# Optimization experiments

Hardware: AMD Instinct MI355X
Metric: run time of the kernel (lower is better)

## Reference

```python
import jax, jax.numpy as jnp
import numpy as np

N = 100_000   # nodes
E = 1_600_000 # edges per edge type
DIN = 128     # input_dim
DH = 128      # prot_hidden_dim
L = 3         # prot_num_layers
EPS = 1e-5


def setup_inputs() -> dict:
    key = jax.random.key(0)
    ks = jax.random.split(key, 8)
    s = 1.0 / np.sqrt(DH)
    return {
        "x": jax.random.normal(ks[0], (N, DIN), jnp.float32),
        "src": jax.random.randint(ks[1], (3, E), 0, N, jnp.int32),
        "dst": jax.random.randint(ks[2], (3, E), 0, N, jnp.int32),
        "gc_W0": jax.random.normal(ks[3], (3, DIN, DH), jnp.float32) * s,
        "gc_b0": jnp.zeros((3, DH), jnp.float32),
        "gc_W": jax.random.normal(ks[4], (L - 1, 3, DH, DH), jnp.float32) * s,
        "gc_b": jnp.zeros((L - 1, 3, DH), jnp.float32),
        "fc_W": jax.random.normal(ks[5], (L, DH, DH), jnp.float32) * s,
        "fc_b": jnp.zeros((L, DH), jnp.float32),
        "bn_gamma": jnp.ones((L, DH), jnp.float32),
        "bn_beta": jnp.zeros((L, DH), jnp.float32),
    }


def _graph_conv(x, src, dst, W, b):
    # DGL GraphConv, norm='both': D_in^{-1/2} A D_out^{-1/2} X W + b
    ones = jnp.ones(src.shape[0], x.dtype)
    deg_out = jnp.clip(jax.ops.segment_sum(ones, src, num_segments=N), 1.0)
    deg_in = jnp.clip(jax.ops.segment_sum(ones, dst, num_segments=N), 1.0)
    # apply weight first (same math; keeps gathered message width = DH)
    h = (x * jax.lax.rsqrt(deg_out)[:, None]) @ W  # [N, DH]
    agg = jax.ops.segment_sum(h[src], dst, num_segments=N)  # gather + scatter-add
    return agg * jax.lax.rsqrt(deg_in)[:, None] + b


def _batchnorm(x, gamma, beta):
    # training-mode BatchNorm1d: biased batch statistics
    mu = jnp.mean(x, axis=0)
    var = jnp.mean(jnp.square(x - mu), axis=0)
    return (x - mu) * jax.lax.rsqrt(var + EPS) * gamma + beta


def reference(x, src, dst, gc_W0, gc_b0, gc_W, gc_b, fc_W, fc_b, bn_gamma, bn_beta):
    h = x
    for l in range(L):
        W = gc_W0 if l == 0 else gc_W[l - 1]
        b = gc_b0 if l == 0 else gc_b[l - 1]
        # HeteroGraphConv with aggregate='sum' over 3 edge types
        out = _graph_conv(h, src[0], dst[0], W[0], b[0])
        for e in range(1, 3):
            out = out + _graph_conv(h, src[e], dst[e], W[e], b[e])
        # FC -> ReLU -> BatchNorm (dropout = identity in eval mode)
        h = _batchnorm(jax.nn.relu(out @ fc_W[l] + fc_b[l]), bn_gamma[l], bn_beta[l])
    return h
```

## Files before the change

### kernel.cpp

```cpp
#include <hip/hip_runtime.h>


#define EPSV 1e-5f
#define CH 4096
#define MAXNB 512

typedef __attribute__((ext_vector_type(8))) short s8v;
typedef __attribute__((ext_vector_type(4))) float f4v;

__global__ void coarse_hist(const int* __restrict__ src, const int* __restrict__ dst,
                            int* __restrict__ chd, int* __restrict__ chs,
                            int E, int NB) {
    __shared__ int hd[MAXNB], hs[MAXNB];
    int t = blockIdx.y;
    for (int i = threadIdx.x; i < MAXNB; i += 256) { hd[i] = 0; hs[i] = 0; }
    __syncthreads();
    int base = blockIdx.x * CH;
    int end = base + CH < E ? base + CH : E;
    const int* sp = src + (size_t)t * E;
    const int* dp = dst + (size_t)t * E;
    for (int i = base + threadIdx.x; i < end; i += 256) {
        atomicAdd(&hd[dp[i] >> 8], 1);
        atomicAdd(&hs[sp[i] >> 8], 1);
    }
    __syncthreads();
    for (int b = threadIdx.x; b < NB; b += 256) {
        if (hd[b]) atomicAdd(&chd[t * NB + b], hd[b]);
        if (hs[b]) atomicAdd(&chs[t * NB + b], hs[b]);
    }
}

__global__ void scan_off(const int* __restrict__ chd, const int* __restrict__ chs,
                         int* __restrict__ offd, int* __restrict__ offs,
                         int* __restrict__ gcd, int* __restrict__ gcs,
                         int* __restrict__ rowptr, int NB, int N, int E) {
    __shared__ int s[MAXNB];
    int tid = threadIdx.x;
    for (int a = 0; a < 6; ++a) {
        const int* h = (a < 3) ? chd + a * NB : chs + (a - 3) * NB;
        int* off = (a < 3) ? offd + a * (NB + 1) : offs + (a - 3) * (NB + 1);
        int* gc = (a < 3) ? gcd + a * NB : gcs + (a - 3) * NB;
        s[tid] = (tid < NB) ? h[tid] : 0;
        __syncthreads();
        for (int o = 1; o < MAXNB; o <<= 1) {
            int v = (tid >= o) ? s[tid - o] : 0;
            __syncthreads();
            s[tid] += v;
            __syncthreads();
        }
        if (tid < NB) {
            off[tid + 1] = s[tid];
            if (tid == 0) off[0] = 0;
        }
        __syncthreads();
        if (tid < NB) gc[tid] = off[tid];
        __syncthreads();
    }
    if (tid < 3) rowptr[tid * (N + 1) + N] = E;
}

__launch_bounds__(256)
__global__ void scatter_coarse(const int* __restrict__ src, const int* __restrict__ dst,
                               int* __restrict__ gcd, int* __restrict__ gcs,
                               int* __restrict__ dbuf, unsigned char* __restrict__ sbuf,
                               int E, int NB) {
    __shared__ int hd[MAXNB], hs[MAXNB];
    __shared__ int lod[MAXNB], los[MAXNB];
    __shared__ int bd[MAXNB], bs[MAXNB];
    __shared__ int rbi[CH];
    __shared__ unsigned char rbs[CH];
    const int tid = threadIdx.x;
    const int t = blockIdx.y;
    const int base = blockIdx.x * CH;
    const int end = base + CH < E ? base + CH : E;
    const int cnt = end - base;
    const int* sp = src + (size_t)t * E;
    const int* dp = dst + (size_t)t * E;

    for (int i = tid; i < MAXNB; i += 256) { hd[i] = 0; hs[i] = 0; }
    __syncthreads();
    for (int i = base + tid; i < end; i += 256) {
        atomicAdd(&hd[dp[i] >> 8], 1);
        atomicAdd(&hs[sp[i] >> 8], 1);
    }
    __syncthreads();
    for (int b = tid; b < NB; b += 256) {
        bd[b] = hd[b] ? atomicAdd(&gcd[t * NB + b], hd[b]) : 0;
        bs[b] = hs[b] ? atomicAdd(&gcs[t * NB + b], hs[b]) : 0;
    }
    lod[tid] = hd[tid]; lod[tid + 256] = hd[tid + 256];
    los[tid] = hs[tid]; los[tid + 256] = hs[tid + 256];
    __syncthreads();
    for (int o = 1; o < MAXNB; o <<= 1) {
        int a0 = lod[tid], a1 = lod[tid + 256];
        int b0 = los[tid], b1 = los[tid + 256];
        int p0 = (tid >= o) ? lod[tid - o] : 0;
        int p1 = lod[tid + 256 - o];
        int q0 = (tid >= o) ? los[tid - o] : 0;
        int q1 = los[tid + 256 - o];
        __syncthreads();
        lod[tid] = a0 + p0; lod[tid + 256] = a1 + p1;
        los[tid] = b0 + q0; los[tid + 256] = b1 + q1;
        __syncthreads();
    }
    hd[tid] = lod[tid] - hd[tid]; hd[tid + 256] = lod[tid + 256] - hd[tid + 256];
    hs[tid] = los[tid] - hs[tid]; hs[tid + 256] = los[tid + 256] - hs[tid + 256];
    __syncthreads();
    for (int i = base + tid; i < end; i += 256) {
        int sv = sp[i], dv = dp[i];
        int lp = atomicAdd(&hd[dv >> 8], 1);
        rbi[lp] = (sv << 8) | (dv & 255);
        int ls = atomicAdd(&hs[sv >> 8], 1);
        rbs[ls] = (unsigned char)(sv & 255);
    }
    __syncthreads();
    for (int i = tid; i < cnt; i += 256) {
        int lo = 0, hi = NB - 1;
        while (lo < hi) { int mid = (lo + hi) >> 1; if (lod[mid] > i) hi = mid; else lo = mid + 1; }
        int excl = lo ? lod[lo - 1] : 0;
        dbuf[(size_t)t * E + bd[lo] + (i - excl)] = rbi[i];
    }
    for (int i = tid; i < cnt; i += 256) {
        int lo = 0, hi = NB - 1;
        while (lo < hi) { int mid = (lo + hi) >> 1; if (los[mid] > i) hi = mid; else lo = mid + 1; }
        int excl = lo ? los[lo - 1] : 0;
        sbuf[(size_t)t * E + bs[lo] + (i - excl)] = rbs[i];
    }
}

__global__ void fine_src(const unsigned char* __restrict__ sbuf, const int* __restrict__ offs,
                         float* __restrict__ dro, int E, int N, int NB) {
    __shared__ int h[256];
    int b = blockIdx.x, t = blockIdx.y;
    int tid = threadIdx.x;
    h[tid] = 0;
    __syncthreads();
    int beg = offs[t * (NB + 1) + b], end = offs[t * (NB + 1) + b + 1];
    const unsigned char* sp = sbuf + (size_t)t * E;
    for (int i = beg + tid; i < end; i += 256) atomicAdd(&h[sp[i]], 1);
    __syncthreads();
    int node = b * 256 + tid;
    if (node < N) {
        int dg = h[tid] < 1 ? 1 : h[tid];
        dro[(size_t)t * N + node] = rsqrtf((float)dg);
    }
}

#define FDCAP 6656
__global__ void fine_dst(const int* __restrict__ dbuf, const int* __restrict__ offd,
                         const float* __restrict__ dro, int2* __restrict__ esrcw,
                         int* __restrict__ rowptr, float* __restrict__ dri,
                         int E, int N, int NB) {
    __shared__ int h[256], sc[256], cur[256];
    __shared__ int rb[FDCAP];
    int b = blockIdx.x, t = blockIdx.y;
    int tid = threadIdx.x;
    h[tid] = 0;
    __syncthreads();
    int beg = offd[t * (NB + 1) + b], end = offd[t * (NB + 1) + b + 1];
    int cnt = end - beg;
    const int* dp = dbuf + (size_t)t * E;
    const float* drt = dro + (size_t)t * N;
    for (int i = beg + tid; i < end; i += 256) atomicAdd(&h[dp[i] & 255], 1);
    __syncthreads();
    sc[tid] = h[tid];
    __syncthreads();
    for (int o = 1; o < 256; o <<= 1) {
        int v = (tid >= o) ? sc[tid - o] : 0;
        __syncthreads();
        sc[tid] += v;
        __syncthreads();
    }
    int excl = sc[tid] - h[tid];
    cur[tid] = excl;
    int node = b * 256 + tid;
    if (node < N) {
        rowptr[t * (N + 1) + node] = beg + excl;
        int dg = h[tid] < 1 ? 1 : h[tid];
        dri[(size_t)t * N + node] = rsqrtf((float)dg);
    }
    __syncthreads();
    if (cnt <= FDCAP) {
        for (int i = beg + tid; i < end; i += 256) {
            int v = dp[i];
            int p = atomicAdd(&cur[v & 255], 1);
            rb[p] = v >> 8;
        }
        __syncthreads();
        for (int i = tid; i < cnt; i += 256) {
            int sv = rb[i];
            esrcw[(size_t)t * E + beg + i] = make_int2(sv, __float_as_int(drt[sv]));
        }
    } else {
        for (int i = beg + tid; i < end; i += 256) {
            int v = dp[i];
            int sv = v >> 8;
            int p = beg + atomicAdd(&cur[v & 255], 1);
            esrcw[(size_t)t * E + p] = make_int2(sv, __float_as_int(drt[sv]));
        }
    }
}

__device__ __forceinline__ unsigned int bfr(float f) {
    unsigned int u = __float_as_uint(f);
    return (u + 0x7FFFu + ((u >> 16) & 1u)) >> 16;
}
__device__ __forceinline__ unsigned int pack2(float lo, float hi) {
    return bfr(lo) | (bfr(hi) << 16);
}
__device__ __forceinline__ float blo(unsigned int u) { return __uint_as_float(u << 16); }
__device__ __forceinline__ float bhi(unsigned int u) { return __uint_as_float(u & 0xFFFF0000u); }

__global__ void cvt_bf16(const float* __restrict__ h, unsigned short* __restrict__ h2,
                         int total8) {
    int i = blockIdx.x * 256 + threadIdx.x;
    if (i >= total8) return;
    const float4* hp = (const float4*)h + (size_t)i * 2;
    float4 v0 = hp[0], v1 = hp[1];
    uint4 o;
    o.x = pack2(v0.x, v0.y);
    o.y = pack2(v0.z, v0.w);
    o.z = pack2(v1.x, v1.y);
    o.w = pack2(v1.z, v1.w);
    ((uint4*)h2)[i] = o;
}

__global__ void pack_w(const float* __restrict__ gcW0, const float* __restrict__ gcW,
                       const float* __restrict__ fcW, unsigned short* __restrict__ Wg,
                       unsigned short* __restrict__ Wf) {
    int mat = blockIdx.x;
    const float* srcp;
    unsigned short* dstp;
    if (mat < 9) {
        int l = mat / 3, e = mat % 3;
        srcp = (l == 0) ? gcW0 + (size_t)e * 16384
                        : gcW + ((size_t)(l - 1) * 3 + e) * 16384;
        dstp = Wg + (size_t)mat * 16384;
    } else {
        srcp = fcW + (size_t)(mat - 9) * 16384;
        dstp = Wf + (size_t)(mat - 9) * 16384;
    }
    for (int p = threadIdx.x; p < 16384; p += 256) {
        int j = p & 7;
        int ln = (p >> 3) & 63;
        int nt = (p >> 9) & 7;
        int ks = p >> 12;
        int k = ks * 32 + (ln >> 4) * 8 + j;
        int n = nt * 16 + (ln & 15);
        dstp[p] = (unsigned short)bfr(srcp[k * 128 + n]);
    }
}

template <int AFF>
__launch_bounds__(256)
__global__ void agg_kernel(const unsigned short* __restrict__ h2, const int* __restrict__ rowptrB,
                           const int2* __restrict__ esrcwB, const float* __restrict__ driB,
                           const float* __restrict__ bnsum, const float* __restrict__ gamma,
                           const float* __restrict__ beta, float invn,
                           unsigned short* __restrict__ zB, int N, int E) {
    __shared__ float lss[256];
    if (AFF) {
        int tid = threadIdx.x;
        if (tid < 128) {
            float mean = bnsum[tid] * invn;
            float var = bnsum[128 + tid] * invn - mean * mean;
            float sc = gamma[tid] * rsqrtf(var + EPSV);
            lss[tid] = sc;
            lss[128 + tid] = beta[tid] - mean * sc;
        }
        __syncthreads();
    }
    const int e = blockIdx.y;
    const int* rowptr = rowptrB + e * (N + 1);
    const int2* esrcw = esrcwB + (size_t)e * E;
    const float* dri = driB + (size_t)e * N;
    unsigned short* z = zB + (size_t)e * N * 128;

    int idx = blockIdx.x * 256 + threadIdx.x;
    int node = idx >> 4;
    int lq = idx & 15;
    if (node >= N) return;
    int beg = rowptr[node], end = rowptr[node + 1];
    const uint4* hp = (const uint4*)h2 + lq;
    float a0 = 0.f, a1 = 0.f, a2 = 0.f, a3 = 0.f, a4 = 0.f, a5 = 0.f, a6 = 0.f, a7 = 0.f;
    float wacc = 0.f;
    int j = beg;
    for (; j + 8 <= end; j += 8) {
        int2 r[8];
#pragma unroll
        for (int q = 0; q < 8; ++q) r[q] = esrcw[j + q];
        uint4 u[8];
#pragma unroll
        for (int q = 0; q < 8; ++q) u[q] = hp[(size_t)r[q].x * 16];
#pragma unroll
        for (int q = 0; q < 8; ++q) {
            float w = __int_as_float(r[q].y);
            if (AFF) wacc += w;
            a0 += w * blo(u[q].x); a1 += w * bhi(u[q].x);
            a2 += w * blo(u[q].y); a3 += w * bhi(u[q].y);
            a4 += w * blo(u[q].z); a5 += w * bhi(u[q].z);
            a6 += w * blo(u[q].w); a7 += w * bhi(u[q].w);
        }
    }
    for (; j + 4 <= end; j += 4) {
        int2 r[4];
#pragma unroll
        for (int q = 0; q < 4; ++q) r[q] = esrcw[j + q];
        uint4 u[4];
#pragma unroll
        for (int q = 0; q < 4; ++q) u[q] = hp[(size_t)r[q].x * 16];
#pragma unroll
        for (int q = 0; q < 4; ++q) {
            float w = __int_as_float(r[q].y);
            if (AFF) wacc += w;
            a0 += w * blo(u[q].x); a1 += w * bhi(u[q].x);
            a2 += w * blo(u[q].y); a3 += w * bhi(u[q].y);
            a4 += w * blo(u[q].z); a5 += w * bhi(u[q].z);
            a6 += w * blo(u[q].w); a7 += w * bhi(u[q].w);
        }
    }
    for (; j < end; ++j) {
        int2 r0 = esrcw[j];
        float w = __int_as_float(r0.y);
        if (AFF) wacc += w;
        uint4 u0 = hp[(size_t)r0.x * 16];
        a0 += w * blo(u0.x); a1 += w * bhi(u0.x);
        a2 += w * blo(u0.y); a3 += w * bhi(u0.y);
        a4 += w * blo(u0.z); a5 += w * bhi(u0.z);
        a6 += w * blo(u0.w); a7 += w * bhi(u0.w);
    }
    float scl = dri[node];
    if (AFF) {
        const float* ap = &lss[lq * 8];
        const float* bp = &lss[128 + lq * 8];
        a0 = ap[0] * a0 + bp[0] * wacc;
        a1 = ap[1] * a1 + bp[1] * wacc;
        a2 = ap[2] * a2 + bp[2] * wacc;
        a3 = ap[3] * a3 + bp[3] * wacc;
        a4 = ap[4] * a4 + bp[4] * wacc;
        a5 = ap[5] * a5 + bp[5] * wacc;
        a6 = ap[6] * a6 + bp[6] * wacc;
        a7 = ap[7] * a7 + bp[7] * wacc;
    }
    uint4 o;
    o.x = pack2(a0 * scl, a1 * scl);
    o.y = pack2(a2 * scl, a3 * scl);
    o.z = pack2(a4 * scl, a5 * scl);
    o.w = pack2(a6 * scl, a7 * scl);
    ((uint4*)z)[(size_t)node * 16 + lq] = o;
}

__launch_bounds__(256)
__global__ void mfma_gc(const unsigned short* __restrict__ zB,
                        const unsigned short* __restrict__ Wp,
                        const float* __restrict__ b3,
                        unsigned short* __restrict__ C, int M) {
    const int tid = threadIdx.x;
    const int l = tid & 63;
    const int wv = tid >> 6;
    const int wm = wv >> 1, wn = wv & 1;
    const int m0 = blockIdx.x * 128;
    const int lr = l & 15;
    const int lk = (l >> 4) * 8;
    f4v acc[4][4];
#pragma unroll
    for (int i = 0; i < 4; ++i)
#pragma unroll
        for (int j = 0; j < 4; ++j) acc[i][j] = (f4v){0.f, 0.f, 0.f, 0.f};

    int rowb[4];
#pragma unroll
    for (int mt = 0; mt < 4; ++mt) {
        int r = m0 + wm * 64 + mt * 16 + lr;
        rowb[mt] = (r < M) ? r : (M - 1);
    }
#pragma unroll
    for (int e = 0; e < 3; ++e) {
        const unsigned short* zp = zB + (size_t)e * M * 128;
        const unsigned short* wp = Wp + (size_t)e * 16384;
#pragma unroll
        for (int ks = 0; ks < 4; ++ks) {
            s8v a[4], b[4];
#pragma unroll
            for (int mt = 0; mt < 4; ++mt)
                a[mt] = *(const s8v*)(zp + (size_t)rowb[mt] * 128 + ks * 32 + lk);
#pragma unroll
            for (int nt = 0; nt < 4; ++nt)
                b[nt] = *(const s8v*)(wp + ks * 4096 + (wn * 4 + nt) * 512 + l * 8);
#pragma unroll
            for (int mt = 0; mt < 4; ++mt)
#pragma unroll
                for (int nt = 0; nt < 4; ++nt)
                    acc[mt][nt] = __builtin_amdgcn_mfma_f32_16x16x32_bf16(
                        a[mt], b[nt], acc[mt][nt], 0, 0, 0);
        }
    }
    float bs[4];
    int col[4];
#pragma unroll
    for (int nt = 0; nt < 4; ++nt) {
        col[nt] = wn * 64 + nt * 16 + lr;
        bs[nt] = b3[col[nt]] + b3[128 + col[nt]] + b3[256 + col[nt]];
    }
#pragma unroll
    for (int mt = 0; mt < 4; ++mt) {
#pragma unroll
        for (int r = 0; r < 4; ++r) {
            int row = m0 + wm * 64 + mt * 16 + (l >> 4) * 4 + r;
            if (row < M) {
                unsigned short* cp = C + (size_t)row * 128;
#pragma unroll
                for (int nt = 0; nt < 4; ++nt)
                    cp[col[nt]] = (unsigned short)bfr(acc[mt][nt][r] + bs[nt]);
            }
        }
    }
}

template <int MODE>
__launch_bounds__(256)
__global__ void mfma_fc(const unsigned short* __restrict__ A,
                        const unsigned short* __restrict__ Wp,
                        const float* __restrict__ bias,
                        unsigned short* __restrict__ outb, float* __restrict__ outf,
                        float* __restrict__ bnsum, int M) {
    __shared__ float red[256];
    const int tid = threadIdx.x;
    const int l = tid & 63;
    const int wv = tid >> 6;
    const int wm = wv >> 1, wn = wv & 1;
    const int m0 = blockIdx.x * 128;
    const int lr = l & 15;
    const int lk = (l >> 4) * 8;
    f4v acc[4][4];
#pragma unroll
    for (int i = 0; i < 4; ++i)
#pragma unroll
        for (int j = 0; j < 4; ++j) acc[i][j] = (f4v){0.f, 0.f, 0.f, 0.f};

    int rowb[4];
#pragma unroll
    for (int mt = 0; mt < 4; ++mt) {
        int r = m0 + wm * 64 + mt * 16 + lr;
        rowb[mt] = (r < M) ? r : (M - 1);
    }
#pragma unroll
    for (int ks = 0; ks < 4; ++ks) {
        s8v a[4], b[4];
#pragma unroll
        for (int mt = 0; mt < 4; ++mt)
            a[mt] = *(const s8v*)(A + (size_t)rowb[mt] * 128 + ks * 32 + lk);
#pragma unroll
        for (int nt = 0; nt < 4; ++nt)
            b[nt] = *(const s8v*)(Wp + ks * 4096 + (wn * 4 + nt) * 512 + l * 8);
#pragma unroll
        for (int mt = 0; mt < 4; ++mt)
#pragma unroll
            for (int nt = 0; nt < 4; ++nt)
                acc[mt][nt] = __builtin_amdgcn_mfma_f32_16x16x32_bf16(
                    a[mt], b[nt], acc[mt][nt], 0, 0, 0);
    }

    float bv[4], cs[4] = {}, cq[4] = {};
    int col[4];
#pragma unroll
    for (int nt = 0; nt < 4; ++nt) {
        col[nt] = wn * 64 + nt * 16 + lr;
        bv[nt] = bias[col[nt]];
    }
#pragma unroll
    for (int mt = 0; mt < 4; ++mt) {
#pragma unroll
        for (int r = 0; r < 4; ++r) {
            int row = m0 + wm * 64 + mt * 16 + (l >> 4) * 4 + r;
            if (row < M) {
#pragma unroll
                for (int nt = 0; nt < 4; ++nt) {
                    float v = acc[mt][nt][r] + bv[nt];
                    v = v > 0.f ? v : 0.f;
                    cs[nt] += v;
                    cq[nt] += v * v;
                    if (MODE == 0)
                        outb[(size_t)row * 128 + col[nt]] = (unsigned short)bfr(v);
                    else
                        outf[(size_t)row * 128 + col[nt]] = v;
                }
            }
        }
    }
    red[tid] = 0.f;
    __syncthreads();
#pragma unroll
    for (int nt = 0; nt < 4; ++nt) {
        atomicAdd(&red[col[nt]], cs[nt]);
        atomicAdd(&red[128 + col[nt]], cq[nt]);
    }
    __syncthreads();
    if (tid < 128) {
        atomicAdd(&bnsum[tid], red[tid]);
        atomicAdd(&bnsum[128 + tid], red[128 + tid]);
    }
}

__global__ void bn_apply(float* __restrict__ h, const float* __restrict__ bnsum,
                         const float* __restrict__ gamma, const float* __restrict__ beta,
                         float invn, int total4) {
    __shared__ float lss[256];
    int tid = threadIdx.x;
    if (tid < 128) {
        float mean = bnsum[tid] * invn;
        float var = bnsum[128 + tid] * invn - mean * mean;
        float sc = gamma[tid] * rsqrtf(var + EPSV);
        lss[tid] = sc;
        lss[128 + tid] = beta[tid] - mean * sc;
    }
    __syncthreads();
    int i = blockIdx.x * 256 + tid;
    if (i >= total4) return;
    int c4 = (i & 31) * 4;
    float4 sc = *(const float4*)&lss[c4];
    float4 sh = *(const float4*)&lss[128 + c4];
    float4 v = ((float4*)h)[i];
    v.x = v.x * sc.x + sh.x;
    v.y = v.y * sc.y + sh.y;
    v.z = v.z * sc.z + sh.z;
    v.w = v.w * sc.w + sh.w;
    ((float4*)h)[i] = v;
}

extern "C" void kernel_launch(void* const* d_in, const int* in_sizes, int n_in,
                              void* d_out, int out_size, void* d_ws, size_t ws_size,
                              hipStream_t stream) {
    const float* x    = (const float*)d_in[0];
    const int*   src  = (const int*)d_in[1];
    const int*   dst  = (const int*)d_in[2];
    const float* gcW0 = (const float*)d_in[3];
    const float* gcb0 = (const float*)d_in[4];
    const float* gcW  = (const float*)d_in[5];
    const float* gcb  = (const float*)d_in[6];
    const float* fcW  = (const float*)d_in[7];
    const float* fcb  = (const float*)d_in[8];
    const float* bng  = (const float*)d_in[9];
    const float* bnb  = (const float*)d_in[10];
    float* out = (float*)d_out;

    const int N = in_sizes[0] / 128;
    const int E = in_sizes[1] / 3;
    const int NB = (N + 255) / 256;

    char* w = (char*)d_ws;
    auto alloc = [&](size_t bytes) -> char* {
        char* p = w;
        w += (bytes + 255) & ~(size_t)255;
        return p;
    };
    unsigned short* zB    = (unsigned short*)alloc((size_t)3 * N * 128 * 2);
    unsigned short* gcout = (unsigned short*)alloc((size_t)N * 128 * 2);
    unsigned short* h2    = (unsigned short*)alloc((size_t)N * 128 * 2);
    unsigned short* Wg    = (unsigned short*)alloc((size_t)9 * 16384 * 2);
    unsigned short* Wf    = (unsigned short*)alloc((size_t)3 * 16384 * 2);
    int2*  esrcw  = (int2*)alloc((size_t)3 * E * 8);
    int*   rowptr = (int*)alloc((size_t)3 * (N + 1) * 4);
    float* dro    = (float*)alloc((size_t)3 * N * 4);
    float* dri    = (float*)alloc((size_t)3 * N * 4);
    int*   chd    = (int*)alloc((size_t)3 * NB * 4);
    int*   chs    = (int*)alloc((size_t)3 * NB * 4);
    int*   offd   = (int*)alloc((size_t)3 * (NB + 1) * 4);
    int*   offs   = (int*)alloc((size_t)3 * (NB + 1) * 4);
    int*   gcd    = (int*)alloc((size_t)3 * NB * 4);
    int*   gcs    = (int*)alloc((size_t)3 * NB * 4);
    float* bnsum  = (float*)alloc(256 * 4);
    int* dbuf = (int*)zB;
    unsigned char* sbuf = (unsigned char*)gcout;

    hipMemsetAsync(chd, 0, (size_t)3 * NB * 4, stream);
    hipMemsetAsync(chs, 0, (size_t)3 * NB * 4, stream);
    dim3 cg2((E + CH - 1) / CH, 3);
    coarse_hist<<<cg2, 256, 0, stream>>>(src, dst, chd, chs, E, NB);
    scan_off<<<1, MAXNB, 0, stream>>>(chd, chs, offd, offs, gcd, gcs, rowptr, NB, N, E);
    scatter_coarse<<<cg2, 256, 0, stream>>>(src, dst, gcd, gcs, dbuf, sbuf, E, NB);
    dim3 fg(NB, 3);
    fine_src<<<fg, 256, 0, stream>>>(sbuf, offs, dro, E, N, NB);
    fine_dst<<<fg, 256, 0, stream>>>(dbuf, offd, dro, esrcw, rowptr, dri, E, N, NB);

    pack_w<<<12, 256, 0, stream>>>(gcW0, gcW, fcW, Wg, Wf);
    const int cvtGrid = (N * 16 + 255) / 256;
    cvt_bf16<<<cvtGrid, 256, 0, stream>>>(x, h2, N * 16);

    const int gemmGrid = (N + 127) / 128;
    const float invn = 1.0f / (float)N;
    dim3 aggG((N * 16 + 255) / 256, 3);

    for (int l = 0; l < 3; ++l) {
        const float* bl = (l == 0) ? gcb0 : gcb + (size_t)(l - 1) * 3 * 128;
        if (l == 0)
            agg_kernel<0><<<aggG, 256, 0, stream>>>(h2, rowptr, esrcw, dri,
                                                    nullptr, nullptr, nullptr, invn,
                                                    zB, N, E);
        else
            agg_kernel<1><<<aggG, 256, 0, stream>>>(h2, rowptr, esrcw, dri,
                                                    bnsum, bng + (size_t)(l - 1) * 128,
                                                    bnb + (size_t)(l - 1) * 128, invn,
                                                    zB, N, E);
        mfma_gc<<<gemmGrid, 256, 0, stream>>>(zB, Wg + (size_t)l * 3 * 16384, bl, gcout, N);
        hipMemsetAsync(bnsum, 0, 256 * 4, stream);
        if (l < 2)
            mfma_fc<0><<<gemmGrid, 256, 0, stream>>>(gcout, Wf + (size_t)l * 16384,
                                                     fcb + (size_t)l * 128, h2, nullptr,
                                                     bnsum, N);
        else
            mfma_fc<1><<<gemmGrid, 256, 0, stream>>>(gcout, Wf + (size_t)l * 16384,
                                                     fcb + (size_t)l * 128, nullptr, out,
                                                     bnsum, N);
    }
    bn_apply<<<(N * 32 + 255) / 256, 256, 0, stream>>>(out, bnsum, bng + 2 * 128,
                                                       bnb + 2 * 128, invn, N * 32);
}
```

Before: 991.6 us.

## Fuse graph-conv and FC GEMMs via LDS, pack edge records to 32-bit

The separate graph-conv GEMM and FC GEMM kernels are merged into one kernel. The bf16 graph-conv output tile is staged in a swizzled shared-memory buffer, so the gcout round trip through global memory goes away. Edge records shrink from int2 (source index plus float weight) to a single int that packs a 20-bit source index with a 12-bit quantized out-degree weight, halving edge traffic in aggregation. The aggregation loop now unrolls 16 edges per iteration instead of 8. The weight quantization adds approximation error, and the 20-bit index caps nodes at about one million.

```diff
diff --git a/kernel.cpp b/kernel.cpp
--- a/kernel.cpp
+++ b/kernel.cpp
@@ -148,7 +148,7 @@
 
 #define FDCAP 6656
 __global__ void fine_dst(const int* __restrict__ dbuf, const int* __restrict__ offd,
-                         const float* __restrict__ dro, int2* __restrict__ esrcw,
+                         const float* __restrict__ dro, int* __restrict__ erec,
                          int* __restrict__ rowptr, float* __restrict__ dri,
                          int E, int N, int NB) {
     __shared__ int h[256], sc[256], cur[256];
@@ -189,14 +189,16 @@
         __syncthreads();
         for (int i = tid; i < cnt; i += 256) {
             int sv = rb[i];
-            esrcw[(size_t)t * E + beg + i] = make_int2(sv, __float_as_int(drt[sv]));
+            int wq = (int)(drt[sv] * 4095.0f + 0.5f);
+            erec[(size_t)t * E + beg + i] = sv | (wq << 20);
         }
     } else {
         for (int i = beg + tid; i < end; i += 256) {
             int v = dp[i];
             int sv = v >> 8;
+            int wq = (int)(drt[sv] * 4095.0f + 0.5f);
             int p = beg + atomicAdd(&cur[v & 255], 1);
-            esrcw[(size_t)t * E + p] = make_int2(sv, __float_as_int(drt[sv]));
+            erec[(size_t)t * E + p] = sv | (wq << 20);
         }
     }
 }
@@ -254,7 +256,7 @@
 template <int AFF>
 __launch_bounds__(256)
 __global__ void agg_kernel(const unsigned short* __restrict__ h2, const int* __restrict__ rowptrB,
-                           const int2* __restrict__ esrcwB, const float* __restrict__ driB,
+                           const int* __restrict__ erecB, const float* __restrict__ driB,
                            const float* __restrict__ bnsum, const float* __restrict__ gamma,
                            const float* __restrict__ beta, float invn,
                            unsigned short* __restrict__ zB, int N, int E) {
@@ -272,7 +274,7 @@
     }
     const int e = blockIdx.y;
     const int* rowptr = rowptrB + e * (N + 1);
-    const int2* esrcw = esrcwB + (size_t)e * E;
+    const int* erec = erecB + (size_t)e * E;
     const float* dri = driB + (size_t)e * N;
     unsigned short* z = zB + (size_t)e * N * 128;
 
@@ -284,17 +286,19 @@
     const uint4* hp = (const uint4*)h2 + lq;
     float a0 = 0.f, a1 = 0.f, a2 = 0.f, a3 = 0.f, a4 = 0.f, a5 = 0.f, a6 = 0.f, a7 = 0.f;
     float wacc = 0.f;
+    const float IW = 1.0f / 4095.0f;
+
     int j = beg;
-    for (; j + 8 <= end; j += 8) {
-        int2 r[8];
-#pragma unroll
-        for (int q = 0; q < 8; ++q) r[q] = esrcw[j + q];
-        uint4 u[8];
-#pragma unroll
-        for (int q = 0; q < 8; ++q) u[q] = hp[(size_t)r[q].x * 16];
-#pragma unroll
-        for (int q = 0; q < 8; ++q) {
-            float w = __int_as_float(r[q].y);
+    for (; j + 16 <= end; j += 16) {
+        int r[16];
+#pragma unroll
+        for (int q = 0; q < 16; ++q) r[q] = erec[j + q];
+        uint4 u[16];
+#pragma unroll
+        for (int q = 0; q < 16; ++q) u[q] = hp[(size_t)(r[q] & 0xFFFFF) * 16];
+#pragma unroll
+        for (int q = 0; q < 16; ++q) {
+            float w = (float)((unsigned)r[q] >> 20) * IW;
             if (AFF) wacc += w;
             a0 += w * blo(u[q].x); a1 += w * bhi(u[q].x);
             a2 += w * blo(u[q].y); a3 += w * bhi(u[q].y);
@@ -303,15 +307,15 @@
         }
     }
     for (; j + 4 <= end; j += 4) {
-        int2 r[4];
-#pragma unroll
-        for (int q = 0; q < 4; ++q) r[q] = esrcw[j + q];
+        int r[4];
+#pragma unroll
+        for (int q = 0; q < 4; ++q) r[q] = erec[j + q];
         uint4 u[4];
 #pragma unroll
-        for (int q = 0; q < 4; ++q) u[q] = hp[(size_t)r[q].x * 16];
+        for (int q = 0; q < 4; ++q) u[q] = hp[(size_t)(r[q] & 0xFFFFF) * 16];
 #pragma unroll
         for (int q = 0; q < 4; ++q) {
-            float w = __int_as_float(r[q].y);
+            float w = (float)((unsigned)r[q] >> 20) * IW;
             if (AFF) wacc += w;
             a0 += w * blo(u[q].x); a1 += w * bhi(u[q].x);
             a2 += w * blo(u[q].y); a3 += w * bhi(u[q].y);
@@ -320,10 +324,10 @@
         }
     }
     for (; j < end; ++j) {
-        int2 r0 = esrcw[j];
-        float w = __int_as_float(r0.y);
+        int r0 = erec[j];
+        float w = (float)((unsigned)r0 >> 20) * IW;
         if (AFF) wacc += w;
-        uint4 u0 = hp[(size_t)r0.x * 16];
+        uint4 u0 = hp[(size_t)(r0 & 0xFFFFF) * 16];
         a0 += w * blo(u0.x); a1 += w * bhi(u0.x);
         a2 += w * blo(u0.y); a3 += w * bhi(u0.y);
         a4 += w * blo(u0.z); a5 += w * bhi(u0.z);
@@ -350,80 +354,16 @@
     ((uint4*)z)[(size_t)node * 16 + lq] = o;
 }
 
-__launch_bounds__(256)
-__global__ void mfma_gc(const unsigned short* __restrict__ zB,
-                        const unsigned short* __restrict__ Wp,
-                        const float* __restrict__ b3,
-                        unsigned short* __restrict__ C, int M) {
-    const int tid = threadIdx.x;
-    const int l = tid & 63;
-    const int wv = tid >> 6;
-    const int wm = wv >> 1, wn = wv & 1;
-    const int m0 = blockIdx.x * 128;
-    const int lr = l & 15;
-    const int lk = (l >> 4) * 8;
-    f4v acc[4][4];
-#pragma unroll
-    for (int i = 0; i < 4; ++i)
-#pragma unroll
-        for (int j = 0; j < 4; ++j) acc[i][j] = (f4v){0.f, 0.f, 0.f, 0.f};
-
-    int rowb[4];
-#pragma unroll
-    for (int mt = 0; mt < 4; ++mt) {
-        int r = m0 + wm * 64 + mt * 16 + lr;
-        rowb[mt] = (r < M) ? r : (M - 1);
-    }
-#pragma unroll
-    for (int e = 0; e < 3; ++e) {
-        const unsigned short* zp = zB + (size_t)e * M * 128;
-        const unsigned short* wp = Wp + (size_t)e * 16384;
-#pragma unroll
-        for (int ks = 0; ks < 4; ++ks) {
-            s8v a[4], b[4];
-#pragma unroll
-            for (int mt = 0; mt < 4; ++mt)
-                a[mt] = *(const s8v*)(zp + (size_t)rowb[mt] * 128 + ks * 32 + lk);
-#pragma unroll
-            for (int nt = 0; nt < 4; ++nt)
-                b[nt] = *(const s8v*)(wp + ks * 4096 + (wn * 4 + nt) * 512 + l * 8);
-#pragma unroll
-            for (int mt = 0; mt < 4; ++mt)
-#pragma unroll
-                for (int nt = 0; nt < 4; ++nt)
-                    acc[mt][nt] = __builtin_amdgcn_mfma_f32_16x16x32_bf16(
-                        a[mt], b[nt], acc[mt][nt], 0, 0, 0);
-        }
-    }
-    float bs[4];
-    int col[4];
-#pragma unroll
-    for (int nt = 0; nt < 4; ++nt) {
-        col[nt] = wn * 64 + nt * 16 + lr;
-        bs[nt] = b3[col[nt]] + b3[128 + col[nt]] + b3[256 + col[nt]];
-    }
-#pragma unroll
-    for (int mt = 0; mt < 4; ++mt) {
-#pragma unroll
-        for (int r = 0; r < 4; ++r) {
-            int row = m0 + wm * 64 + mt * 16 + (l >> 4) * 4 + r;
-            if (row < M) {
-                unsigned short* cp = C + (size_t)row * 128;
-#pragma unroll
-                for (int nt = 0; nt < 4; ++nt)
-                    cp[col[nt]] = (unsigned short)bfr(acc[mt][nt][r] + bs[nt]);
-            }
-        }
-    }
-}
-
 template <int MODE>
 __launch_bounds__(256)
-__global__ void mfma_fc(const unsigned short* __restrict__ A,
-                        const unsigned short* __restrict__ Wp,
-                        const float* __restrict__ bias,
-                        unsigned short* __restrict__ outb, float* __restrict__ outf,
-                        float* __restrict__ bnsum, int M) {
+__global__ void mfma_layer(const unsigned short* __restrict__ zB,
+                           const unsigned short* __restrict__ Wgp,
+                           const float* __restrict__ b3,
+                           const unsigned short* __restrict__ Wfp,
+                           const float* __restrict__ fcb,
+                           unsigned short* __restrict__ outb, float* __restrict__ outf,
+                           float* __restrict__ bnsum, int M) {
+    __shared__ unsigned short T[128 * 128];
     __shared__ float red[256];
     const int tid = threadIdx.x;
     const int l = tid & 63;
@@ -432,11 +372,6 @@
     const int m0 = blockIdx.x * 128;
     const int lr = l & 15;
     const int lk = (l >> 4) * 8;
-    f4v acc[4][4];
-#pragma unroll
-    for (int i = 0; i < 4; ++i)
-#pragma unroll
-        for (int j = 0; j < 4; ++j) acc[i][j] = (f4v){0.f, 0.f, 0.f, 0.f};
 
     int rowb[4];
 #pragma unroll
@@ -444,21 +379,81 @@
         int r = m0 + wm * 64 + mt * 16 + lr;
         rowb[mt] = (r < M) ? r : (M - 1);
     }
+
+    {
+        f4v acc[4][4];
+#pragma unroll
+        for (int i = 0; i < 4; ++i)
+#pragma unroll
+            for (int j = 0; j < 4; ++j) acc[i][j] = (f4v){0.f, 0.f, 0.f, 0.f};
+#pragma unroll
+        for (int e = 0; e < 3; ++e) {
+            const unsigned short* zp = zB + (size_t)e * M * 128;
+            const unsigned short* wp = Wgp + (size_t)e * 16384;
+#pragma unroll
+            for (int ks = 0; ks < 4; ++ks) {
+                s8v a[4], b[4];
+#pragma unroll
+                for (int mt = 0; mt < 4; ++mt)
+                    a[mt] = *(const s8v*)(zp + (size_t)rowb[mt] * 128 + ks * 32 + lk);
+#pragma unroll
+                for (int nt = 0; nt < 4; ++nt)
+                    b[nt] = *(const s8v*)(wp + ks * 4096 + (wn * 4 + nt) * 512 + l * 8);
+#pragma unroll
+                for (int mt = 0; mt < 4; ++mt)
+#pragma unroll
+                    for (int nt = 0; nt < 4; ++nt)
+                        acc[mt][nt] = __builtin_amdgcn_mfma_f32_16x16x32_bf16(
+                            a[mt], b[nt], acc[mt][nt], 0, 0, 0);
+            }
+        }
+        float bs[4];
+        int col[4];
+#pragma unroll
+        for (int nt = 0; nt < 4; ++nt) {
+            col[nt] = wn * 64 + nt * 16 + lr;
+            bs[nt] = b3[col[nt]] + b3[128 + col[nt]] + b3[256 + col[nt]];
+        }
+#pragma unroll
+        for (int mt = 0; mt < 4; ++mt) {
+#pragma unroll
+            for (int r = 0; r < 4; ++r) {
+                int rl = wm * 64 + mt * 16 + (l >> 4) * 4 + r;
+#pragma unroll
+                for (int nt = 0; nt < 4; ++nt) {
+                    int c = col[nt];
+                    int chunk = (c >> 3) ^ (rl & 15);
+                    T[rl * 128 + chunk * 8 + (c & 7)] =
+                        (unsigned short)bfr(acc[mt][nt][r] + bs[nt]);
+                }
+            }
+        }
+    }
+    __syncthreads();
+
+    f4v acc2[4][4];
+#pragma unroll
+    for (int i = 0; i < 4; ++i)
+#pragma unroll
+        for (int j = 0; j < 4; ++j) acc2[i][j] = (f4v){0.f, 0.f, 0.f, 0.f};
 #pragma unroll
     for (int ks = 0; ks < 4; ++ks) {
         s8v a[4], b[4];
 #pragma unroll
+        for (int mt = 0; mt < 4; ++mt) {
+            int rl = wm * 64 + mt * 16 + lr;
+            int chunk = (ks * 4 + (l >> 4)) ^ lr;
+            a[mt] = *(const s8v*)&T[rl * 128 + chunk * 8];
+        }
+#pragma unroll
+        for (int nt = 0; nt < 4; ++nt)
+            b[nt] = *(const s8v*)(Wfp + ks * 4096 + (wn * 4 + nt) * 512 + l * 8);
+#pragma unroll
         for (int mt = 0; mt < 4; ++mt)
-            a[mt] = *(const s8v*)(A + (size_t)rowb[mt] * 128 + ks * 32 + lk);
-#pragma unroll
-        for (int nt = 0; nt < 4; ++nt)
-            b[nt] = *(const s8v*)(Wp + ks * 4096 + (wn * 4 + nt) * 512 + l * 8);
-#pragma unroll
-        for (int mt = 0; mt < 4; ++mt)
 #pragma unroll
             for (int nt = 0; nt < 4; ++nt)
-                acc[mt][nt] = __builtin_amdgcn_mfma_f32_16x16x32_bf16(
-                    a[mt], b[nt], acc[mt][nt], 0, 0, 0);
+                acc2[mt][nt] = __builtin_amdgcn_mfma_f32_16x16x32_bf16(
+                    a[mt], b[nt], acc2[mt][nt], 0, 0, 0);
     }
 
     float bv[4], cs[4] = {}, cq[4] = {};
@@ -466,7 +461,7 @@
 #pragma unroll
     for (int nt = 0; nt < 4; ++nt) {
         col[nt] = wn * 64 + nt * 16 + lr;
-        bv[nt] = bias[col[nt]];
+        bv[nt] = fcb[col[nt]];
     }
 #pragma unroll
     for (int mt = 0; mt < 4; ++mt) {
@@ -476,7 +471,7 @@
             if (row < M) {
 #pragma unroll
                 for (int nt = 0; nt < 4; ++nt) {
-                    float v = acc[mt][nt][r] + bv[nt];
+                    float v = acc2[mt][nt][r] + bv[nt];
                     v = v > 0.f ? v : 0.f;
                     cs[nt] += v;
                     cq[nt] += v * v;
@@ -555,11 +550,10 @@
         return p;
     };
     unsigned short* zB    = (unsigned short*)alloc((size_t)3 * N * 128 * 2);
-    unsigned short* gcout = (unsigned short*)alloc((size_t)N * 128 * 2);
     unsigned short* h2    = (unsigned short*)alloc((size_t)N * 128 * 2);
     unsigned short* Wg    = (unsigned short*)alloc((size_t)9 * 16384 * 2);
     unsigned short* Wf    = (unsigned short*)alloc((size_t)3 * 16384 * 2);
-    int2*  esrcw  = (int2*)alloc((size_t)3 * E * 8);
+    int*   erec   = (int*)alloc((size_t)3 * E * 4);
     int*   rowptr = (int*)alloc((size_t)3 * (N + 1) * 4);
     float* dro    = (float*)alloc((size_t)3 * N * 4);
     float* dri    = (float*)alloc((size_t)3 * N * 4);
@@ -571,7 +565,7 @@
     int*   gcs    = (int*)alloc((size_t)3 * NB * 4);
     float* bnsum  = (float*)alloc(256 * 4);
     int* dbuf = (int*)zB;
-    unsigned char* sbuf = (unsigned char*)gcout;
+    unsigned char* sbuf = (unsigned char*)(dbuf + (size_t)3 * E);
 
     hipMemsetAsync(chd, 0, (size_t)3 * NB * 4, stream);
     hipMemsetAsync(chs, 0, (size_t)3 * NB * 4, stream);
@@ -581,7 +575,7 @@
     scatter_coarse<<<cg2, 256, 0, stream>>>(src, dst, gcd, gcs, dbuf, sbuf, E, NB);
     dim3 fg(NB, 3);
     fine_src<<<fg, 256, 0, stream>>>(sbuf, offs, dro, E, N, NB);
-    fine_dst<<<fg, 256, 0, stream>>>(dbuf, offd, dro, esrcw, rowptr, dri, E, N, NB);
+    fine_dst<<<fg, 256, 0, stream>>>(dbuf, offd, dro, erec, rowptr, dri, E, N, NB);
 
     pack_w<<<12, 256, 0, stream>>>(gcW0, gcW, fcW, Wg, Wf);
     const int cvtGrid = (N * 16 + 255) / 256;
@@ -594,24 +588,25 @@
     for (int l = 0; l < 3; ++l) {
         const float* bl = (l == 0) ? gcb0 : gcb + (size_t)(l - 1) * 3 * 128;
         if (l == 0)
-            agg_kernel<0><<<aggG, 256, 0, stream>>>(h2, rowptr, esrcw, dri,
+            agg_kernel<0><<<aggG, 256, 0, stream>>>(h2, rowptr, erec, dri,
                                                     nullptr, nullptr, nullptr, invn,
                                                     zB, N, E);
         else
-            agg_kernel<1><<<aggG, 256, 0, stream>>>(h2, rowptr, esrcw, dri,
+            agg_kernel<1><<<aggG, 256, 0, stream>>>(h2, rowptr, erec, dri,
                                                     bnsum, bng + (size_t)(l - 1) * 128,
                                                     bnb + (size_t)(l - 1) * 128, invn,
                                                     zB, N, E);
-        mfma_gc<<<gemmGrid, 256, 0, stream>>>(zB, Wg + (size_t)l * 3 * 16384, bl, gcout, N);
         hipMemsetAsync(bnsum, 0, 256 * 4, stream);
         if (l < 2)
-            mfma_fc<0><<<gemmGrid, 256, 0, stream>>>(gcout, Wf + (size_t)l * 16384,
-                                                     fcb + (size_t)l * 128, h2, nullptr,
-                                                     bnsum, N);
+            mfma_layer<0><<<gemmGrid, 256, 0, stream>>>(zB, Wg + (size_t)l * 3 * 16384, bl,
+                                                        Wf + (size_t)l * 16384,
+                                                        fcb + (size_t)l * 128,
+                                                        h2, nullptr, bnsum, N);
         else
-            mfma_fc<1><<<gemmGrid, 256, 0, stream>>>(gcout, Wf + (size_t)l * 16384,
-                                                     fcb + (size_t)l * 128, nullptr, out,
-                                                     bnsum, N);
+            mfma_layer<1><<<gemmGrid, 256, 0, stream>>>(zB, Wg + (size_t)l * 3 * 16384, bl,
+                                                        Wf + (size_t)l * 16384,
+                                                        fcb + (size_t)l * 128,
+                                                        nullptr, out, bnsum, N);
     }
     bn_apply<<<(N * 32 + 255) / 256, 256, 0, stream>>>(out, bnsum, bng + 2 * 128,
                                                        bnb + 2 * 128, invn, N * 32);
```

Result: faster. 927.8 us (-6.4%).
